# Kernel optimization log

Measured on AMD Instinct MI355X. Metric: run time of the kernel, lower is better.

## Reference

```python
import jax, jax.numpy as jnp
import numpy as np

N_NODES = 100000
N_EDGES = 3200000
D_IN = 128


def setup_inputs() -> dict:
    key = jax.random.key(0)
    k1, k2, k3, k4 = jax.random.split(key, 4)
    x = jax.random.normal(k1, (N_NODES, D_IN), dtype=jnp.float32)
    edge_index = jax.random.randint(k2, (2, N_EDGES), 0, N_NODES, dtype=jnp.int64)
    W1 = jax.random.normal(k3, (D_IN, 16), dtype=jnp.float32) * (1.0 / np.sqrt(D_IN))
    b1 = jnp.zeros((16,), dtype=jnp.float32)
    W2 = jax.random.normal(k4, (16, 2), dtype=jnp.float32) * (1.0 / np.sqrt(16))
    b2 = jnp.zeros((2,), dtype=jnp.float32)
    return {"x": x, "edge_index": edge_index, "W1": W1, "b1": b1, "W2": W2, "b2": b2}


def _gcn_norm(edge_index, n_nodes):
    # Add self-loops, then symmetric degree normalization (PyG gcn_norm).
    loops = jnp.arange(n_nodes, dtype=edge_index.dtype)
    row = jnp.concatenate([edge_index[0], loops])  # source
    col = jnp.concatenate([edge_index[1], loops])  # target
    ones = jnp.ones(row.shape[0], dtype=jnp.float32)
    deg = jax.ops.segment_sum(ones, col, num_segments=n_nodes)
    dis = jnp.where(deg > 0, jax.lax.rsqrt(deg), 0.0)  # deg^{-1/2}
    norm = dis[row] * dis[col]  # [E+N]
    return row, col, norm


def _gcn_conv(x, row, col, norm, W, b, n_nodes):
    h = x @ W  # transform first (PyG order): [N, out]
    msgs = h[row] * norm[:, None]  # gather from source, scale
    agg = jax.ops.segment_sum(msgs, col, num_segments=n_nodes)  # scatter-add to target
    return agg + b


def reference(x, edge_index, W1, b1, W2, b2):
    n = x.shape[0]
    row, col, norm = _gcn_norm(edge_index, n)
    h = _gcn_conv(x, row, col, norm, W1, b1, n)
    h = jax.nn.relu(h)
    h = _gcn_conv(h, row, col, norm, W2, b2, n)
    return jax.nn.log_softmax(h, axis=1)
```

## Files before the change

kernel.cpp:

```cpp
#include <hip/hip_runtime.h>
#include <hip/hip_fp16.h>

#define DIN 128
#define BSH 7
#define BSIZE 128
#define NBMAX 800
#define CAP 4480
#define CHUNK 6656
#define EPT 13
#define PB 512
#define HR 128
#define XSTR 136
#define PZ 0xAAAAAAAAu

typedef _Float16 half8_t __attribute__((ext_vector_type(8)));
typedef _Float16 half4_t __attribute__((ext_vector_type(4)));
typedef float f32x4_t __attribute__((ext_vector_type(4)));

struct PlaceSmem {
    int pk[CHUNK];
    unsigned short bkid[CHUNK];
    int lcnt[NBMAX], lstart[NBMAX], gofs[NBMAX], lcur[NBMAX];
    int sst[16];
};
struct HSmem {
    _Float16 xh[HR * XSTR];
};
union __align__(16) MegaSmem {
    PlaceSmem p;
    HSmem h;
};

__global__ __launch_bounds__(PB, 6) void mega_kernel(const int* __restrict__ row,
                                                     const int* __restrict__ col,
                                                     const float* __restrict__ x,
                                                     const float* __restrict__ W1,
                                                     unsigned* __restrict__ cur,
                                                     int* __restrict__ sp,
                                                     __half* __restrict__ hp,
                                                     int E, int N, int NB, int PBLKS) {
    __shared__ MegaSmem sm;
    int t = threadIdx.x;
    int bid = blockIdx.x;

    if (bid < PBLKS) {
        int e0 = bid * CHUNK;
        int cnt = min(CHUNK, E - e0);
        bool full = (cnt == CHUNK);
        for (int i = t; i < NBMAX; i += PB) { sm.p.lcnt[i] = 0; sm.p.lcur[i] = 0; }
        __syncthreads();
        int cv[EPT], rv[EPT];
        if (full) {
            #pragma unroll
            for (int k = 0; k < EPT; k++) cv[k] = col[e0 + t + k * PB];
            #pragma unroll
            for (int k = 0; k < EPT; k++) rv[k] = row[e0 + t + k * PB];
            #pragma unroll
            for (int k = 0; k < EPT; k++) atomicAdd(&sm.p.lcnt[cv[k] >> BSH], 1);
        } else {
            for (int i = t; i < cnt; i += PB)
                atomicAdd(&sm.p.lcnt[col[e0 + i] >> BSH], 1);
        }
        __syncthreads();
        int b2i = t * 2;
        int v0 = (b2i + 0 < NBMAX) ? sm.p.lcnt[b2i + 0] : 0;
        int v1 = (b2i + 1 < NBMAX) ? sm.p.lcnt[b2i + 1] : 0;
        unsigned g0 = 0, g1 = 0;
        if (b2i + 0 < NB && v0) g0 = atomicAdd(&cur[b2i + 0], (unsigned)v0) - PZ;
        if (b2i + 1 < NB && v1) g1 = atomicAdd(&cur[b2i + 1], (unsigned)v1) - PZ;
        int tot = v0 + v1;
        int lane = t & 63, w = t >> 6;
        int sc = tot;
        #pragma unroll
        for (int d = 1; d < 64; d <<= 1) {
            int up = __shfl_up(sc, d);
            if (lane >= d) sc += up;
        }
        if (lane == 63) sm.p.sst[w] = sc;
        __syncthreads();
        if (t < 64) {
            int v = (lane < 8) ? sm.p.sst[lane] : 0;
            #pragma unroll
            for (int d = 1; d < 8; d <<= 1) {
                int up = __shfl_up(v, d);
                if (lane >= d) v += up;
            }
            if (lane < 8) sm.p.sst[8 + lane] = v;
        }
        __syncthreads();
        int wpre = (w > 0) ? sm.p.sst[8 + w - 1] : 0;
        int ex = sc + wpre - tot;
        if (b2i + 0 < NBMAX) sm.p.lstart[b2i + 0] = ex;
        if (b2i + 1 < NBMAX) sm.p.lstart[b2i + 1] = ex + v0;
        if (b2i + 0 < NB) sm.p.gofs[b2i + 0] = (b2i + 0) * CAP + (int)g0 - ex;
        if (b2i + 1 < NB) sm.p.gofs[b2i + 1] = (b2i + 1) * CAP + (int)g1 - (ex + v0);
        __syncthreads();
        if (full) {
            #pragma unroll
            for (int k = 0; k < EPT; k++) {
                int cc = cv[k];
                int b  = cc >> BSH;
                int rk = atomicAdd(&sm.p.lcur[b], 1);
                int pos = sm.p.lstart[b] + rk;
                sm.p.pk[pos]   = ((cc & (BSIZE - 1)) << 17) | rv[k];
                sm.p.bkid[pos] = (unsigned short)b;
            }
            __syncthreads();
            #pragma unroll
            for (int k = 0; k < EPT; k++) {
                int i = t + k * PB;
                sp[sm.p.gofs[sm.p.bkid[i]] + i] = sm.p.pk[i];
            }
        } else {
            for (int i = t; i < cnt; i += PB) {
                int r  = row[e0 + i];
                int cc = col[e0 + i];
                int b  = cc >> BSH;
                int rk = atomicAdd(&sm.p.lcur[b], 1);
                int pos = sm.p.lstart[b] + rk;
                sm.p.pk[pos]   = ((cc & (BSIZE - 1)) << 17) | r;
                sm.p.bkid[pos] = (unsigned short)b;
            }
            __syncthreads();
            for (int i = t; i < cnt; i += PB)
                sp[sm.p.gofs[sm.p.bkid[i]] + i] = sm.p.pk[i];
        }
    } else {
        int base = (bid - PBLKS) * HR;
        _Float16* xh = sm.h.xh;
        int nrow = min(HR, N - base);
        int lane = t & 63, w = t >> 6;
        int cl = lane & 15;
        int kg = (lane >> 4) * 8;
        half8_t bf[4];
        #pragma unroll
        for (int s = 0; s < 4; s++) {
            #pragma unroll
            for (int i = 0; i < 8; i++)
                bf[s][i] = (_Float16)W1[(s * 32 + kg + i) * 16 + cl];
        }
        #pragma unroll
        for (int q = 0; q < 8; q++) {
            int idx = q * 512 + t;
            int r = idx >> 5, c4 = idx & 31;
            float4 v = make_float4(0.f, 0.f, 0.f, 0.f);
            if (r < nrow) v = *(const float4*)(x + (size_t)(base + r) * DIN + c4 * 4);
            half4_t h4;
            h4[0] = (_Float16)v.x; h4[1] = (_Float16)v.y;
            h4[2] = (_Float16)v.z; h4[3] = (_Float16)v.w;
            *(half4_t*)(xh + r * XSTR + c4 * 4) = h4;
        }
        __syncthreads();
        int mb = w * 16;
        const _Float16* xr = xh + (mb + cl) * XSTR;
        f32x4_t acc = {0.f, 0.f, 0.f, 0.f};
        #pragma unroll
        for (int s = 0; s < 4; s++) {
            half8_t af = *(const half8_t*)(xr + kg + s * 32);
            acc = __builtin_amdgcn_mfma_f32_16x16x32_f16(af, bf[s], acc, 0, 0, 0);
        }
        int m0 = mb + (lane >> 4) * 4;
        #pragma unroll
        for (int r = 0; r < 4; r++) {
            int n = base + m0 + r;
            if (n < N) hp[(size_t)n * 16 + cl] = __float2half((float)acc[r]);
        }
    }
}

__global__ __launch_bounds__(512) void sort_kernel(const int* __restrict__ sp,
                                                   const unsigned* __restrict__ cur,
                                                   int* __restrict__ srt2,
                                                   int* __restrict__ off,
                                                   __half* __restrict__ hp, int N) {
    __shared__ int ss[CAP];
    __shared__ int lcnt[BSIZE], lstart[BSIZE], lcur[BSIZE];
    __shared__ float disl[BSIZE];
    __shared__ int stot[2];
    int B = blockIdx.x;
    int t = threadIdx.x;
    int cntb = (int)(cur[B] - PZ);
    const int* reg = sp + (size_t)B * CAP;
    if (t < BSIZE) { lcnt[t] = 0; lcur[t] = 0; }
    __syncthreads();
    int rc[9];
    #pragma unroll
    for (int k = 0; k < 9; k++) {
        int i = k * 512 + t;
        rc[k] = (i < cntb) ? reg[i] : -1;
    }
    #pragma unroll
    for (int k = 0; k < 9; k++)
        if (rc[k] >= 0) atomicAdd(&lcnt[rc[k] >> 17], 1);
    __syncthreads();
    int lane = t & 63, w = t >> 6;
    int v = (t < BSIZE) ? lcnt[t] : 0;
    int sc = v;
    #pragma unroll
    for (int d = 1; d < 64; d <<= 1) {
        int up = __shfl_up(sc, d);
        if (lane >= d) sc += up;
    }
    if (t < BSIZE && lane == 63) stot[w] = sc;
    __syncthreads();
    if (t < BSIZE) {
        lstart[t] = sc - v + ((w == 1) ? stot[0] : 0);
        disl[t] = rsqrtf((float)v + 1.0f);
    }
    __syncthreads();
    #pragma unroll
    for (int k = 0; k < 9; k++) {
        int vv = rc[k];
        if (vv >= 0) {
            int lc = vv >> 17;
            int rk = atomicAdd(&lcur[lc], 1);
            ss[lstart[lc] + rk] = vv & 0x1FFFF;
        }
    }
    __syncthreads();
    for (int i = t; i < cntb; i += 512) srt2[(size_t)B * CAP + i] = ss[i];
    if (t < BSIZE) {
        off[B * (BSIZE + 1) + t] = B * CAP + lstart[t];
    } else if (t == BSIZE) {
        off[B * (BSIZE + 1) + BSIZE] = B * CAP + cntb;
    }
    int r = t >> 2, part = t & 3;
    int gt = B * BSIZE + r;
    if (gt < N) {
        uint2* p = (uint2*)(hp + (size_t)gt * 16) + part;
        uint2 vv = *p;
        __half2* h2 = (__half2*)&vv;
        float dv = disl[r];
        #pragma unroll
        for (int q = 0; q < 2; q++) {
            float2 f = __half22float2(h2[q]);
            f.x *= dv; f.y *= dv;
            h2[q] = __float22half2_rn(f);
        }
        *p = vv;
    }
}

__global__ __launch_bounds__(512) void g1_kernel(const int* __restrict__ srt2,
                                                 const int* __restrict__ off,
                                                 const unsigned* __restrict__ cur,
                                                 const __half* __restrict__ hp,
                                                 const float* __restrict__ b1,
                                                 const float* __restrict__ W2,
                                                 float* __restrict__ gp, int N) {
    __shared__ int ss[CAP];
    int B = blockIdx.x;
    int t = threadIdx.x;
    int cntb = (int)(cur[B] - PZ);
    for (int i = t; i < cntb; i += 512) ss[i] = srt2[(size_t)B * CAP + i];
    __syncthreads();
    const uint2* hp4 = (const uint2*)hp;
    int k2  = t & 3;
    int grp = t >> 2;
    int gt = B * BSIZE + grp;
    if (gt >= N) return;
    int j0 = off[B * (BSIZE + 1) + grp] - B * CAP;
    int j1 = off[B * (BSIZE + 1) + grp + 1] - B * CAP;
    float d = rsqrtf((float)(j1 - j0) + 1.0f);
    uint2 sq = hp4[(size_t)gt * 4 + k2];
    float2 a0 = __half22float2(((__half2*)&sq)[0]);
    float2 a1 = __half22float2(((__half2*)&sq)[1]);
    float2 b0 = make_float2(0.f, 0.f), b1v = make_float2(0.f, 0.f);
    float2 c0 = make_float2(0.f, 0.f), c1 = make_float2(0.f, 0.f);
    float2 e0 = make_float2(0.f, 0.f), e1 = make_float2(0.f, 0.f);
    int j = j0;
    for (; j + 3 < j1; j += 4) {
        int r0 = ss[j + 0], r1 = ss[j + 1], r2 = ss[j + 2], r3 = ss[j + 3];
        uint2 q0 = hp4[(size_t)r0 * 4 + k2];
        uint2 q1 = hp4[(size_t)r1 * 4 + k2];
        uint2 q2 = hp4[(size_t)r2 * 4 + k2];
        uint2 q3 = hp4[(size_t)r3 * 4 + k2];
        float2 f;
        f = __half22float2(((__half2*)&q0)[0]); a0.x += f.x; a0.y += f.y;
        f = __half22float2(((__half2*)&q0)[1]); a1.x += f.x; a1.y += f.y;
        f = __half22float2(((__half2*)&q1)[0]); b0.x += f.x; b0.y += f.y;
        f = __half22float2(((__half2*)&q1)[1]); b1v.x += f.x; b1v.y += f.y;
        f = __half22float2(((__half2*)&q2)[0]); c0.x += f.x; c0.y += f.y;
        f = __half22float2(((__half2*)&q2)[1]); c1.x += f.x; c1.y += f.y;
        f = __half22float2(((__half2*)&q3)[0]); e0.x += f.x; e0.y += f.y;
        f = __half22float2(((__half2*)&q3)[1]); e1.x += f.x; e1.y += f.y;
    }
    for (; j < j1; j++) {
        int r = ss[j];
        uint2 q = hp4[(size_t)r * 4 + k2];
        float2 f;
        f = __half22float2(((__half2*)&q)[0]); a0.x += f.x; a0.y += f.y;
        f = __half22float2(((__half2*)&q)[1]); a1.x += f.x; a1.y += f.y;
    }
    a0.x += b0.x + c0.x + e0.x;  a0.y += b0.y + c0.y + e0.y;
    a1.x += b1v.x + c1.x + e1.x; a1.y += b1v.y + c1.y + e1.y;
    int k0 = k2 * 4;
    float v0 = fmaxf(fmaf(a0.x, d, b1[k0 + 0]), 0.0f);
    float v1 = fmaxf(fmaf(a0.y, d, b1[k0 + 1]), 0.0f);
    float v2 = fmaxf(fmaf(a1.x, d, b1[k0 + 2]), 0.0f);
    float v3 = fmaxf(fmaf(a1.y, d, b1[k0 + 3]), 0.0f);
    float p0 = v0 * W2[(k0 + 0) * 2 + 0] + v1 * W2[(k0 + 1) * 2 + 0]
             + v2 * W2[(k0 + 2) * 2 + 0] + v3 * W2[(k0 + 3) * 2 + 0];
    float p1 = v0 * W2[(k0 + 0) * 2 + 1] + v1 * W2[(k0 + 1) * 2 + 1]
             + v2 * W2[(k0 + 2) * 2 + 1] + v3 * W2[(k0 + 3) * 2 + 1];
    p0 += __shfl_xor(p0, 1); p1 += __shfl_xor(p1, 1);
    p0 += __shfl_xor(p0, 2); p1 += __shfl_xor(p1, 2);
    if (k2 == 0) *(float2*)(gp + (size_t)gt * 2) = make_float2(p0 * d, p1 * d);
}

__global__ __launch_bounds__(256) void g2_kernel(const int* __restrict__ srt2,
                                                 const int* __restrict__ off,
                                                 const float* __restrict__ gp,
                                                 const float* __restrict__ b2,
                                                 float* __restrict__ out, int N) {
    int t = blockIdx.x * 256 + threadIdx.x;
    int c    = t >> 3;
    int slot = t & 7;
    if (c >= N) return;
    int idx = (c >> 7) * (BSIZE + 1) + (c & 127);
    int j0 = off[idx];
    int j1 = off[idx + 1];
    float a0 = 0.0f, a1v = 0.0f;
    float c0 = 0.0f, c1v = 0.0f;
    int j = j0 + slot;
    for (; j + 24 < j1; j += 32) {
        int r0 = srt2[j];
        int r1 = srt2[j + 8];
        int r2 = srt2[j + 16];
        int r3 = srt2[j + 24];
        float2 g0 = *(const float2*)(gp + (size_t)r0 * 2);
        float2 g1 = *(const float2*)(gp + (size_t)r1 * 2);
        float2 g2 = *(const float2*)(gp + (size_t)r2 * 2);
        float2 g3 = *(const float2*)(gp + (size_t)r3 * 2);
        a0  += g0.x + g2.x;  a1v += g0.y + g2.y;
        c0  += g1.x + g3.x;  c1v += g1.y + g3.y;
    }
    for (; j < j1; j += 8) {
        int r = srt2[j];
        float2 gv = *(const float2*)(gp + (size_t)r * 2);
        a0  += gv.x;
        a1v += gv.y;
    }
    a0 += c0; a1v += c1v;
    a0 += __shfl_xor(a0, 1); a1v += __shfl_xor(a1v, 1);
    a0 += __shfl_xor(a0, 2); a1v += __shfl_xor(a1v, 2);
    a0 += __shfl_xor(a0, 4); a1v += __shfl_xor(a1v, 4);
    if (slot == 0) {
        float2 self = *(const float2*)(gp + (size_t)c * 2);
        float d = rsqrtf((float)(j1 - j0) + 1.0f);
        float o0 = (a0  + self.x) * d + b2[0];
        float o1 = (a1v + self.y) * d + b2[1];
        float m = fmaxf(o0, o1);
        float lse = m + logf(expf(o0 - m) + expf(o1 - m));
        *(float2*)(out + (size_t)c * 2) = make_float2(o0 - lse, o1 - lse);
    }
}

extern "C" void kernel_launch(void* const* d_in, const int* in_sizes, int n_in,
                              void* d_out, int out_size, void* d_ws, size_t ws_size,
                              hipStream_t stream) {
    const float* x  = (const float*)d_in[0];
    const int*   ei = (const int*)d_in[1];
    const float* W1 = (const float*)d_in[2];
    const float* b1 = (const float*)d_in[3];
    const float* W2 = (const float*)d_in[4];
    const float* b2 = (const float*)d_in[5];
    float* out = (float*)d_out;

    const int N = in_sizes[0] / DIN;
    const int E = in_sizes[1] / 2;
    const int* row = ei;
    const int* col = ei + E;
    const int NB    = (N + BSIZE - 1) / BSIZE;
    const int PBLKS = (E + CHUNK - 1) / CHUNK;
    const int HBLKS = (N + HR - 1) / HR;

    unsigned* cur  = (unsigned*)d_ws;
    int*      off  = (int*)(cur + NBMAX);
    int*      sp   = off + (size_t)NBMAX * (BSIZE + 1);
    int*      srt2 = sp + (size_t)NBMAX * CAP;
    __half*   hp   = (__half*)(srt2 + (size_t)NBMAX * CAP);
    float*    gp   = (float*)(hp + (size_t)N * 16);

    mega_kernel <<<PBLKS + HBLKS, PB, 0, stream>>>(row, col, x, W1, cur, sp, hp, E, N, NB, PBLKS);
    sort_kernel <<<NB, 512, 0, stream>>>(sp, cur, srt2, off, hp, N);
    g1_kernel   <<<NB, 512, 0, stream>>>(srt2, off, cur, (const __half*)hp, b1, W2, gp, N);
    g2_kernel   <<<(int)(((size_t)N * 8 + 255) / 256), 256, 0, stream>>>(srt2, off, gp, b2, out, N);
}
```

Baseline: 180.3 us.

## Fuse sort, layer-1 gather and layer-2 gather into one cooperative kernel

Replaces the three kernels that ran after the mega kernel (sort, g1, g2) with a single cooperative launch that uses grid.sync between phases. Each block keeps its sorted source list in shared memory across all phases, so the sorted-index and offset arrays no longer round-trip through global memory and two launches go away. The layer-2 gather is now done by 4 threads per node inside the block instead of a separate grid. Correctness relies on the whole grid of NB blocks being co-resident (about 782 blocks of 512 threads), and the code falls back to the old three-kernel path if the cooperative launch fails.

```diff
diff --git a/kernel.cpp b/kernel.cpp
--- a/kernel.cpp
+++ b/kernel.cpp
@@ -1,5 +1,8 @@
 #include <hip/hip_runtime.h>
 #include <hip/hip_fp16.h>
+#include <hip/hip_cooperative_groups.h>
+
+namespace cg = cooperative_groups;
 
 #define DIN 128
 #define BSH 7
@@ -164,6 +167,168 @@
         for (int r = 0; r < 4; r++) {
             int n = base + m0 + r;
             if (n < N) hp[(size_t)n * 16 + cl] = __float2half((float)acc[r]);
+        }
+    }
+}
+
+__global__ __launch_bounds__(512, 8) void fused_kernel(const int* __restrict__ sp,
+                                                       const unsigned* __restrict__ cur,
+                                                       __half* __restrict__ hp,
+                                                       const float* __restrict__ b1,
+                                                       const float* __restrict__ W2,
+                                                       const float* __restrict__ b2,
+                                                       float* __restrict__ gp,
+                                                       float* __restrict__ out, int N) {
+    cg::grid_group grid = cg::this_grid();
+    __shared__ int ss[CAP];
+    __shared__ int lcnt[BSIZE], lstart[BSIZE], lcur[BSIZE];
+    __shared__ int stot[2];
+    int B = blockIdx.x;
+    int t = threadIdx.x;
+    int cntb = (int)(cur[B] - PZ);
+    const int* reg = sp + (size_t)B * CAP;
+    if (t < BSIZE) { lcnt[t] = 0; lcur[t] = 0; }
+    __syncthreads();
+    int rc[9];
+    #pragma unroll
+    for (int k = 0; k < 9; k++) {
+        int i = k * 512 + t;
+        rc[k] = (i < cntb) ? reg[i] : -1;
+    }
+    #pragma unroll
+    for (int k = 0; k < 9; k++)
+        if (rc[k] >= 0) atomicAdd(&lcnt[rc[k] >> 17], 1);
+    __syncthreads();
+    int lane = t & 63, w = t >> 6;
+    int v = (t < BSIZE) ? lcnt[t] : 0;
+    int sc = v;
+    #pragma unroll
+    for (int d = 1; d < 64; d <<= 1) {
+        int up = __shfl_up(sc, d);
+        if (lane >= d) sc += up;
+    }
+    if (t < BSIZE && lane == 63) stot[w] = sc;
+    __syncthreads();
+    if (t < BSIZE) lstart[t] = sc - v + ((w == 1) ? stot[0] : 0);
+    __syncthreads();
+    #pragma unroll
+    for (int k = 0; k < 9; k++) {
+        int vv = rc[k];
+        if (vv >= 0) {
+            int lc = vv >> 17;
+            int rk = atomicAdd(&lcur[lc], 1);
+            ss[lstart[lc] + rk] = vv & 0x1FFFF;
+        }
+    }
+    {
+        int r = t >> 2, part = t & 3;
+        int gt = B * BSIZE + r;
+        if (gt < N) {
+            float dv = rsqrtf((float)lcnt[r] + 1.0f);
+            uint2* p = (uint2*)(hp + (size_t)gt * 16) + part;
+            uint2 vv = *p;
+            __half2* h2 = (__half2*)&vv;
+            #pragma unroll
+            for (int q = 0; q < 2; q++) {
+                float2 f = __half22float2(h2[q]);
+                f.x *= dv; f.y *= dv;
+                h2[q] = __float22half2_rn(f);
+            }
+            *p = vv;
+        }
+    }
+    __threadfence();
+    grid.sync();
+
+    int k2  = t & 3;
+    int grp = t >> 2;
+    int gt  = B * BSIZE + grp;
+    bool valid = (gt < N);
+    int j0 = valid ? lstart[grp] : 0;
+    int j1 = valid ? (j0 + lcnt[grp]) : 0;
+    float d = rsqrtf((float)(j1 - j0) + 1.0f);
+    float2 myg = make_float2(0.f, 0.f);
+    {
+        const uint2* hp4 = (const uint2*)hp;
+        float2 a0 = make_float2(0.f, 0.f), a1 = make_float2(0.f, 0.f);
+        if (valid) {
+            uint2 sq = hp4[(size_t)gt * 4 + k2];
+            a0 = __half22float2(((__half2*)&sq)[0]);
+            a1 = __half22float2(((__half2*)&sq)[1]);
+        }
+        float2 b0 = make_float2(0.f, 0.f), b1v = make_float2(0.f, 0.f);
+        float2 c0 = make_float2(0.f, 0.f), c1 = make_float2(0.f, 0.f);
+        float2 e0 = make_float2(0.f, 0.f), e1 = make_float2(0.f, 0.f);
+        int j = j0;
+        for (; j + 3 < j1; j += 4) {
+            int r0 = ss[j + 0], r1 = ss[j + 1], r2 = ss[j + 2], r3 = ss[j + 3];
+            uint2 q0 = hp4[(size_t)r0 * 4 + k2];
+            uint2 q1 = hp4[(size_t)r1 * 4 + k2];
+            uint2 q2 = hp4[(size_t)r2 * 4 + k2];
+            uint2 q3 = hp4[(size_t)r3 * 4 + k2];
+            float2 f;
+            f = __half22float2(((__half2*)&q0)[0]); a0.x += f.x; a0.y += f.y;
+            f = __half22float2(((__half2*)&q0)[1]); a1.x += f.x; a1.y += f.y;
+            f = __half22float2(((__half2*)&q1)[0]); b0.x += f.x; b0.y += f.y;
+            f = __half22float2(((__half2*)&q1)[1]); b1v.x += f.x; b1v.y += f.y;
+            f = __half22float2(((__half2*)&q2)[0]); c0.x += f.x; c0.y += f.y;
+            f = __half22float2(((__half2*)&q2)[1]); c1.x += f.x; c1.y += f.y;
+            f = __half22float2(((__half2*)&q3)[0]); e0.x += f.x; e0.y += f.y;
+            f = __half22float2(((__half2*)&q3)[1]); e1.x += f.x; e1.y += f.y;
+        }
+        for (; j < j1; j++) {
+            int r = ss[j];
+            uint2 q = hp4[(size_t)r * 4 + k2];
+            float2 f;
+            f = __half22float2(((__half2*)&q)[0]); a0.x += f.x; a0.y += f.y;
+            f = __half22float2(((__half2*)&q)[1]); a1.x += f.x; a1.y += f.y;
+        }
+        a0.x += b0.x + c0.x + e0.x;  a0.y += b0.y + c0.y + e0.y;
+        a1.x += b1v.x + c1.x + e1.x; a1.y += b1v.y + c1.y + e1.y;
+        int k0 = k2 * 4;
+        float v0 = fmaxf(fmaf(a0.x, d, b1[k0 + 0]), 0.0f);
+        float v1 = fmaxf(fmaf(a0.y, d, b1[k0 + 1]), 0.0f);
+        float v2 = fmaxf(fmaf(a1.x, d, b1[k0 + 2]), 0.0f);
+        float v3 = fmaxf(fmaf(a1.y, d, b1[k0 + 3]), 0.0f);
+        float p0 = v0 * W2[(k0 + 0) * 2 + 0] + v1 * W2[(k0 + 1) * 2 + 0]
+                 + v2 * W2[(k0 + 2) * 2 + 0] + v3 * W2[(k0 + 3) * 2 + 0];
+        float p1 = v0 * W2[(k0 + 0) * 2 + 1] + v1 * W2[(k0 + 1) * 2 + 1]
+                 + v2 * W2[(k0 + 2) * 2 + 1] + v3 * W2[(k0 + 3) * 2 + 1];
+        p0 += __shfl_xor(p0, 1); p1 += __shfl_xor(p1, 1);
+        p0 += __shfl_xor(p0, 2); p1 += __shfl_xor(p1, 2);
+        myg = make_float2(p0 * d, p1 * d);
+        if (valid && k2 == 0) *(float2*)(gp + (size_t)gt * 2) = myg;
+    }
+    __threadfence();
+    grid.sync();
+
+    {
+        float2 a = make_float2(0.f, 0.f), b = make_float2(0.f, 0.f);
+        float2 c = make_float2(0.f, 0.f), e = make_float2(0.f, 0.f);
+        int j = j0 + k2;
+        for (; j + 12 < j1; j += 16) {
+            int r0 = ss[j], r1 = ss[j + 4], r2 = ss[j + 8], r3 = ss[j + 12];
+            float2 g0 = *(const float2*)(gp + (size_t)r0 * 2);
+            float2 g1 = *(const float2*)(gp + (size_t)r1 * 2);
+            float2 g2 = *(const float2*)(gp + (size_t)r2 * 2);
+            float2 g3 = *(const float2*)(gp + (size_t)r3 * 2);
+            a.x += g0.x; a.y += g0.y;  b.x += g1.x; b.y += g1.y;
+            c.x += g2.x; c.y += g2.y;  e.x += g3.x; e.y += g3.y;
+        }
+        for (; j < j1; j += 4) {
+            int r = ss[j];
+            float2 gv = *(const float2*)(gp + (size_t)r * 2);
+            a.x += gv.x; a.y += gv.y;
+        }
+        a.x += b.x + c.x + e.x;  a.y += b.y + c.y + e.y;
+        a.x += __shfl_xor(a.x, 1); a.y += __shfl_xor(a.y, 1);
+        a.x += __shfl_xor(a.x, 2); a.y += __shfl_xor(a.y, 2);
+        if (valid && k2 == 0) {
+            float o0 = (a.x + myg.x) * d + b2[0];
+            float o1 = (a.y + myg.y) * d + b2[1];
+            float m = fmaxf(o0, o1);
+            float lse = m + logf(expf(o0 - m) + expf(o1 - m));
+            *(float2*)(out + (size_t)gt * 2) = make_float2(o0 - lse, o1 - lse);
         }
     }
 }
@@ -383,7 +548,19 @@
     float*    gp   = (float*)(hp + (size_t)N * 16);
 
     mega_kernel <<<PBLKS + HBLKS, PB, 0, stream>>>(row, col, x, W1, cur, sp, hp, E, N, NB, PBLKS);
-    sort_kernel <<<NB, 512, 0, stream>>>(sp, cur, srt2, off, hp, N);
-    g1_kernel   <<<NB, 512, 0, stream>>>(srt2, off, cur, (const __half*)hp, b1, W2, gp, N);
-    g2_kernel   <<<(int)(((size_t)N * 8 + 255) / 256), 256, 0, stream>>>(srt2, off, gp, b2, out, N);
+
+    {
+        const int* sp_ = sp; const unsigned* cur_ = cur; __half* hp_ = hp;
+        const float* b1_ = b1; const float* W2_ = W2; const float* b2_ = b2;
+        float* gp_ = gp; float* out_ = out; int n_ = N;
+        void* kargs[] = {(void*)&sp_, (void*)&cur_, (void*)&hp_, (void*)&b1_,
+                         (void*)&W2_, (void*)&b2_, (void*)&gp_, (void*)&out_, (void*)&n_};
+        hipError_t err = hipLaunchCooperativeKernel((const void*)fused_kernel,
+                                                    dim3(NB), dim3(512), kargs, 0, stream);
+        if (err != hipSuccess) {
+            sort_kernel <<<NB, 512, 0, stream>>>(sp, cur, srt2, off, hp, N);
+            g1_kernel   <<<NB, 512, 0, stream>>>(srt2, off, cur, (const __half*)hp, b1, W2, gp, N);
+            g2_kernel   <<<(int)(((size_t)N * 8 + 255) / 256), 256, 0, stream>>>(srt2, off, gp, b2, out, N);
+        }
+    }
 }
```

Measured after the change: 541.8 us. 3x slower.
